# Performance work log

Hardware: AMD Instinct MI355X
Metric: run time of the kernel (lower is better)

The kernel has to match this reference:

```python
import jax, jax.numpy as jnp
import numpy as np

SEQ, D, H, FF = 2048, 1024, 16, 4096
HD = D // H  # head_dim = 64


def setup_inputs() -> dict:
    key = jax.random.key(0)
    ks = jax.random.split(key, 13)
    s = lambda k, shape, fan_in: jax.random.normal(k, shape, jnp.float32) / np.sqrt(fan_in)
    return {
        "x":  jax.random.normal(ks[0], (SEQ, D), jnp.float32),
        # per-head Q/K/V linears, batched over the head axis: [H, D, HD]
        "Wq": s(ks[1], (H, D, HD), D), "bq": jnp.zeros((H, HD), jnp.float32),
        "Wk": s(ks[2], (H, D, HD), D), "bk": jnp.zeros((H, HD), jnp.float32),
        "Wv": s(ks[3], (H, D, HD), D), "bv": jnp.zeros((H, HD), jnp.float32),
        "Wp": s(ks[4], (D, D), D),     "bp": jnp.zeros((D,), jnp.float32),
        "W1": s(ks[5], (D, FF), D),    "b1": jnp.zeros((FF,), jnp.float32),
        "W2": s(ks[6], (FF, D), FF),   "b2": jnp.zeros((D,), jnp.float32),
    }


def reference(x, Wq, bq, Wk, bk, Wv, bv, Wp, bp, W1, b1, W2, b2):
    # Batched per-head projections: [H, S, HD]
    Qx = jnp.einsum("sd,hde->hse", x, Wq) + bq[:, None, :]
    Kx = jnp.einsum("sd,hde->hse", x, Wk) + bk[:, None, :]
    Vx = jnp.einsum("sd,hde->hse", x, Wv) + bv[:, None, :]
    # scores[h,s,t] = Qx[h,s]. Kx[h,t] / sqrt(HD); softmax over t (last dim)
    scores = jnp.einsum("hse,hte->hst", Qx, Kx) / jnp.sqrt(jnp.float32(HD))
    attn = jax.nn.softmax(scores, axis=-1)
    # Faithful to source: head[t,e] = sum_s Vx[s,e] * attn[s,t]  (attn^T @ V)
    heads = jnp.einsum("hse,hst->hte", Vx, attn)  # [H, S, HD]
    # concat heads along feature dim (head-major order) -> [S, D]
    concat = jnp.transpose(heads, (1, 0, 2)).reshape(SEQ, H * HD)
    proj = concat @ Wp + bp
    hidden = jax.nn.relu(proj @ W1 + b1)
    out = hidden @ W2 + b2
    return out
```

## Files before the change

### kernel.cpp

```cpp
#include <hip/hip_runtime.h>
#include <math.h>

constexpr int S_  = 2048;
constexpr int D_  = 1024;
constexpr int H_  = 16;
constexpr int HD_ = 64;
constexpr int FF_ = 4096;

typedef short bf16x8 __attribute__((ext_vector_type(8)));
typedef float f32x4  __attribute__((ext_vector_type(4)));

static __device__ __forceinline__ ushort f2bf(float f) {
    unsigned x = __float_as_uint(f);
    unsigned r = (x + 0x7fffu + ((x >> 16) & 1u)) >> 16;
    return (ushort)r;
}
static __device__ __forceinline__ float bf2f(ushort u) {
    return __uint_as_float(((unsigned)u) << 16);
}

static __device__ __forceinline__ void gload_lds16(const void* g, void* l) {
    __builtin_amdgcn_global_load_lds(
        (const __attribute__((address_space(1))) unsigned int*)g,
        (__attribute__((address_space(3))) unsigned int*)l, 16, 0, 0);
}

__global__ __launch_bounds__(256) void cast_f32_bf16(
    const float* __restrict__ in, ushort* __restrict__ out, int n)
{
    int i = (blockIdx.x * 256 + threadIdx.x) * 4;
    if (i < n) {
        float4 v = *(const float4*)(in + i);
        ushort4 o;
        o.x = f2bf(v.x); o.y = f2bf(v.y); o.z = f2bf(v.z); o.w = f2bf(v.w);
        *(ushort4*)(out + i) = o;
    }
}

__global__ __launch_bounds__(256) void transpose_cast(
    const float* __restrict__ in, ushort* __restrict__ out,
    int K, int N, long inZ, long outZ)
{
    const float* B = in + (size_t)blockIdx.z * inZ;
    ushort* BT = out + (size_t)blockIdx.z * outZ;
    __shared__ float Ts[32][33];
    const int n0 = blockIdx.x * 32, k0 = blockIdx.y * 32;
    const int r = threadIdx.x >> 3, c4 = (threadIdx.x & 7) * 4;
    float4 v = *(const float4*)(B + (size_t)(k0 + r) * N + n0 + c4);
    Ts[r][c4 + 0] = v.x; Ts[r][c4 + 1] = v.y;
    Ts[r][c4 + 2] = v.z; Ts[r][c4 + 3] = v.w;
    __syncthreads();
    ushort4 o;
    o.x = f2bf(Ts[c4 + 0][r]); o.y = f2bf(Ts[c4 + 1][r]);
    o.z = f2bf(Ts[c4 + 2][r]); o.w = f2bf(Ts[c4 + 3][r]);
    *(ushort4*)(BT + (size_t)(n0 + r) * K + k0 + c4) = o;
}

__global__ __launch_bounds__(256) void bias_cat(
    const float* __restrict__ bq, const float* __restrict__ bk,
    const float* __restrict__ bv, float* __restrict__ out)
{
    int i = blockIdx.x * 256 + threadIdx.x;
    float v = (i < 1024) ? bq[i] : (i < 2048 ? bk[i - 1024] : bv[i - 2048]);
    out[i] = v;
}

template <int BM, int BN, int WR, int WC, int KS, int RELU, int OUT>
__global__ __launch_bounds__(WR * WC * 64) void gemm_mfma(
    const ushort* __restrict__ A, const ushort* __restrict__ BT,
    const float* __restrict__ bias, void* __restrict__ Cv,
    void* __restrict__ Cv2, int M, int N, int K)
{
    constexpr int WAVES = WR * WC;
    constexpr int WTM = BM / WR, WTN = BN / WC;
    constexpr int MT = WTM / 16, NT = WTN / 16;
    constexpr int AI = BM / 16;
    constexpr int TI = (BM + BN) / 16;
    constexpr int PW = TI / WAVES;

    __shared__ ushort As[BM * 32];
    __shared__ ushort Bs[BN * 32];

    const int tid = threadIdx.x;
    const int lane = tid & 63;
    const int wave = tid >> 6;
    const int wr = wave / WC, wc = wave % WC;
    const int row16 = lane & 15, kgrp = lane >> 4;
    const int m0 = blockIdx.y * BM, n0 = blockIdx.x * BN;
    const int kOff = blockIdx.z * (K / KS);

    const int lrow = lane >> 2;
    const int gcol8 = (lane & 3) ^ (lrow & 3);
    const int aslot = kgrp ^ (row16 & 3);

    f32x4 acc[MT][NT];
#pragma unroll
    for (int i = 0; i < MT; ++i)
#pragma unroll
        for (int j = 0; j < NT; ++j) acc[i][j] = (f32x4){0.f, 0.f, 0.f, 0.f};

    for (int k0 = kOff; k0 < kOff + K / KS; k0 += 32) {
        __syncthreads();
#pragma unroll
        for (int i = 0; i < PW; ++i) {
            const int inst = wave * PW + i;
            if (inst < AI) {
                const int row = inst * 16 + lrow;
                gload_lds16(A + (size_t)(m0 + row) * K + k0 + gcol8 * 8,
                            As + row * 32 + (lane & 3) * 8);
            } else {
                const int row = (inst - AI) * 16 + lrow;
                gload_lds16(BT + (size_t)(n0 + row) * K + k0 + gcol8 * 8,
                            Bs + row * 32 + (lane & 3) * 8);
            }
        }
        __syncthreads();

        bf16x8 af[MT], bfr[NT];
#pragma unroll
        for (int mt = 0; mt < MT; ++mt)
            af[mt] = *(const bf16x8*)(As + (wr * WTM + mt * 16 + row16) * 32 + aslot * 8);
#pragma unroll
        for (int nt = 0; nt < NT; ++nt)
            bfr[nt] = *(const bf16x8*)(Bs + (wc * WTN + nt * 16 + row16) * 32 + aslot * 8);
#pragma unroll
        for (int mt = 0; mt < MT; ++mt)
#pragma unroll
            for (int nt = 0; nt < NT; ++nt)
                acc[mt][nt] = __builtin_amdgcn_mfma_f32_16x16x32_bf16(
                    af[mt], bfr[nt], acc[mt][nt], 0, 0, 0);
    }

    if constexpr (OUT == 2) {
        float* Cp = ((blockIdx.z < KS / 2) ? (float*)Cv : (float*)Cv2)
                    + (size_t)(blockIdx.z % (KS / 2)) * M * N;
#pragma unroll
        for (int nt = 0; nt < NT; ++nt) {
            const int n = n0 + wc * WTN + nt * 16 + row16;
#pragma unroll
            for (int mt = 0; mt < MT; ++mt)
#pragma unroll
                for (int r = 0; r < 4; ++r) {
                    const int m = m0 + wr * WTM + mt * 16 + kgrp * 4 + r;
                    Cp[(size_t)m * N + n] = acc[mt][nt][r];
                }
        }
    } else if constexpr (OUT == 3) {
        ushort* QKo = (ushort*)Cv;
        ushort* VTo = (ushort*)Cv2;
        if (n0 < 2048) {
#pragma unroll
            for (int nt = 0; nt < NT; ++nt) {
                const int n = n0 + wc * WTN + nt * 16 + row16;
                const float bb = bias[n];
#pragma unroll
                for (int mt = 0; mt < MT; ++mt)
#pragma unroll
                    for (int r = 0; r < 4; ++r) {
                        const int m = m0 + wr * WTM + mt * 16 + kgrp * 4 + r;
                        QKo[(size_t)m * 2048 + n] = f2bf(acc[mt][nt][r] + bb);
                    }
            }
        } else {
#pragma unroll
            for (int nt = 0; nt < NT; ++nt) {
                const int n = n0 + wc * WTN + nt * 16 + row16;
                const float bb = bias[n];
#pragma unroll
                for (int mt = 0; mt < MT; ++mt) {
                    const int mb = m0 + wr * WTM + mt * 16 + kgrp * 4;
                    ushort4 o;
                    o.x = f2bf(acc[mt][nt][0] + bb);
                    o.y = f2bf(acc[mt][nt][1] + bb);
                    o.z = f2bf(acc[mt][nt][2] + bb);
                    o.w = f2bf(acc[mt][nt][3] + bb);
                    *(ushort4*)(VTo + (size_t)(n - 2048) * 2048 + mb) = o;
                }
            }
        }
    } else {
#pragma unroll
        for (int nt = 0; nt < NT; ++nt) {
            const int n = n0 + wc * WTN + nt * 16 + row16;
            const float bb = bias ? bias[n] : 0.f;
#pragma unroll
            for (int mt = 0; mt < MT; ++mt)
#pragma unroll
                for (int r = 0; r < 4; ++r) {
                    const int m = m0 + wr * WTM + mt * 16 + kgrp * 4 + r;
                    float v = acc[mt][nt][r] + bb;
                    if (RELU) v = fmaxf(v, 0.f);
                    if (OUT == 1)
                        ((ushort*)Cv)[(size_t)m * N + n] = f2bf(v);
                    else
                        ((float*)Cv)[(size_t)m * N + n] = v;
                }
        }
    }
}

__global__ __launch_bounds__(256) void reduce4_bias(
    const float* __restrict__ pA, const float* __restrict__ pB,
    const float* __restrict__ bias, float* __restrict__ out, int MN, int N)
{
    const int i = (blockIdx.x * 256 + threadIdx.x) * 4;
    float4 a = *(const float4*)(pA + i);
    const float4 b = *(const float4*)(pA + (size_t)MN + i);
    const float4 c = *(const float4*)(pB + i);
    const float4 d = *(const float4*)(pB + (size_t)MN + i);
    const float4 e = *(const float4*)(bias + (i & (N - 1)));
    a.x += b.x + c.x + d.x + e.x;
    a.y += b.y + c.y + d.y + e.y;
    a.z += b.z + c.z + d.z + e.z;
    a.w += b.w + c.w + d.w + e.w;
    *(float4*)(out + i) = a;
}

__global__ __launch_bounds__(256) void attn_stats(
    const ushort* __restrict__ QK, float* __restrict__ part)
{
    const int h = blockIdx.y;
    const int s0 = blockIdx.x * 128;
    const int tz = blockIdx.z;
    const int tid = threadIdx.x;
    const int lane = tid & 63;
    const int w = tid >> 6;
    const int row16 = lane & 15;
    const int kgrp = lane >> 4;

    __shared__ ushort Ks[64 * 64];

    bf16x8 qf[2][2];
#pragma unroll
    for (int mt = 0; mt < 2; ++mt) {
        const ushort* qp = QK + (size_t)(s0 + w * 32 + mt * 16 + row16) * 2048 + h * 64;
        qf[mt][0] = *(const bf16x8*)(qp + kgrp * 8);
        qf[mt][1] = *(const bf16x8*)(qp + kgrp * 8 + 32);
    }

    float suml[2][4] = {{0.f}};
    const int r0 = tid >> 3, c0 = tid & 7;
    const int sl = (c0 ^ (r0 & 7)) * 8;

    for (int ti = 0; ti < 8; ++ti) {
        const int t0 = tz * 512 + ti * 64;
        uint4 ka = *(const uint4*)(QK + (size_t)(t0 + r0) * 2048 + 1024 + h * 64 + c0 * 8);
        uint4 kb = *(const uint4*)(QK + (size_t)(t0 + 32 + r0) * 2048 + 1024 + h * 64 + c0 * 8);
        __syncthreads();
        *(uint4*)(Ks + r0 * 64 + sl) = ka;
        *(uint4*)(Ks + (r0 + 32) * 64 + sl) = kb;
        __syncthreads();
#pragma unroll
        for (int nt = 0; nt < 4; ++nt) {
            const int kr = nt * 16 + row16;
            bf16x8 kf0 = *(const bf16x8*)(Ks + kr * 64 + ((kgrp ^ (kr & 7)) * 8));
            bf16x8 kf1 = *(const bf16x8*)(Ks + kr * 64 + (((kgrp + 4) ^ (kr & 7)) * 8));
#pragma unroll
            for (int mt = 0; mt < 2; ++mt) {
                f32x4 sc = (f32x4){0.f, 0.f, 0.f, 0.f};
                sc = __builtin_amdgcn_mfma_f32_16x16x32_bf16(qf[mt][0], kf0, sc, 0, 0, 0);
                sc = __builtin_amdgcn_mfma_f32_16x16x32_bf16(qf[mt][1], kf1, sc, 0, 0, 0);
#pragma unroll
                for (int r = 0; r < 4; ++r)
                    suml[mt][r] += __expf(sc[r] * 0.125f);
            }
        }
    }
#pragma unroll
    for (int mt = 0; mt < 2; ++mt)
#pragma unroll
        for (int r = 0; r < 4; ++r) {
#pragma unroll
            for (int m = 1; m < 16; m <<= 1)
                suml[mt][r] += __shfl_xor(suml[mt][r], m, 64);
        }
    if (row16 == 0) {
#pragma unroll
        for (int mt = 0; mt < 2; ++mt)
#pragma unroll
            for (int r = 0; r < 4; ++r)
                part[((size_t)tz * H_ + h) * S_ + s0 + w * 32 + mt * 16 + kgrp * 4 + r]
                    = suml[mt][r];
    }
}

__global__ __launch_bounds__(256) void make_invL(
    const float* __restrict__ part, float* __restrict__ invL)
{
    const int i = blockIdx.x * 256 + threadIdx.x;
    const int HS = H_ * S_;
    float s = part[i] + part[HS + i] + part[2 * HS + i] + part[3 * HS + i];
    invL[i] = 1.f / s;
}

__global__ __launch_bounds__(256) void vscale(
    ushort* __restrict__ VT, const float* __restrict__ invL)
{
    const int r = blockIdx.x;
    const int c = threadIdx.x * 8;
    const float* il = invL + (r >> 6) * S_ + c;
    union { uint4 u; ushort s[8]; } v;
    v.u = *(const uint4*)(VT + (size_t)r * S_ + c);
    float4 l0 = *(const float4*)(il);
    float4 l1 = *(const float4*)(il + 4);
    v.s[0] = f2bf(bf2f(v.s[0]) * l0.x);
    v.s[1] = f2bf(bf2f(v.s[1]) * l0.y);
    v.s[2] = f2bf(bf2f(v.s[2]) * l0.z);
    v.s[3] = f2bf(bf2f(v.s[3]) * l0.w);
    v.s[4] = f2bf(bf2f(v.s[4]) * l1.x);
    v.s[5] = f2bf(bf2f(v.s[5]) * l1.y);
    v.s[6] = f2bf(bf2f(v.s[6]) * l1.z);
    v.s[7] = f2bf(bf2f(v.s[7]) * l1.w);
    *(uint4*)(VT + (size_t)r * S_ + c) = v.u;
}

__global__ __launch_bounds__(256) void attn_pv(
    const ushort* __restrict__ QK, const ushort* __restrict__ VT,
    ushort* __restrict__ pvp)
{
    const int h = blockIdx.y;
    const int t0 = blockIdx.x * 128;
    const int sbase = blockIdx.z * 512;
    const int tid = threadIdx.x;
    const int lane = tid & 63;
    const int w = tid >> 6;
    const int row16 = lane & 15;
    const int kgrp = lane >> 4;

    __shared__ ushort KP[128 * 64];
    __shared__ ushort Qs[64 * 64];
    __shared__ ushort Vs[64 * 64];

    const int r0 = tid >> 3, c0 = tid & 7;
    const int sl = (c0 ^ (r0 & 7)) * 8;

#pragma unroll
    for (int i = 0; i < 4; ++i) {
        const int r = r0 + i * 32;
        uint4 kv = *(const uint4*)(QK + (size_t)(t0 + r) * 2048 + 1024 + h * 64 + c0 * 8);
        *(uint4*)(KP + r * 64 + sl) = kv;
    }
    __syncthreads();
    bf16x8 kf[8][2];
#pragma unroll
    for (int nt = 0; nt < 8; ++nt) {
        const int r = nt * 16 + row16;
        kf[nt][0] = *(const bf16x8*)(KP + r * 64 + ((kgrp ^ (r & 7)) * 8));
        kf[nt][1] = *(const bf16x8*)(KP + r * 64 + (((kgrp + 4) ^ (r & 7)) * 8));
    }

    f32x4 acc[2][4];
#pragma unroll
    for (int i = 0; i < 2; ++i)
#pragma unroll
        for (int j = 0; j < 4; ++j) acc[i][j] = (f32x4){0.f, 0.f, 0.f, 0.f};

    for (int si = 0; si < 8; ++si) {
        const int s0 = sbase + si * 64;
        uint4 qa = *(const uint4*)(QK + (size_t)(s0 + r0) * 2048 + h * 64 + c0 * 8);
        uint4 qb = *(const uint4*)(QK + (size_t)(s0 + 32 + r0) * 2048 + h * 64 + c0 * 8);
        uint4 va = *(const uint4*)(VT + (size_t)(h * 64 + r0) * 2048 + s0 + c0 * 8);
        uint4 vb = *(const uint4*)(VT + (size_t)(h * 64 + 32 + r0) * 2048 + s0 + c0 * 8);
        __syncthreads();
        *(uint4*)(Qs + r0 * 64 + sl) = qa;
        *(uint4*)(Qs + (r0 + 32) * 64 + sl) = qb;
        *(uint4*)(Vs + r0 * 64 + sl) = va;
        *(uint4*)(Vs + (r0 + 32) * 64 + sl) = vb;
        __syncthreads();

        const int qr = w * 16 + row16;
        bf16x8 qf0 = *(const bf16x8*)(Qs + qr * 64 + ((kgrp ^ (qr & 7)) * 8));
        bf16x8 qf1 = *(const bf16x8*)(Qs + qr * 64 + (((kgrp + 4) ^ (qr & 7)) * 8));
#pragma unroll
        for (int nt = 0; nt < 8; ++nt) {
            f32x4 sc = (f32x4){0.f, 0.f, 0.f, 0.f};
            sc = __builtin_amdgcn_mfma_f32_16x16x32_bf16(qf0, kf[nt][0], sc, 0, 0, 0);
            sc = __builtin_amdgcn_mfma_f32_16x16x32_bf16(qf1, kf[nt][1], sc, 0, 0, 0);
            ushort4 o;
            o.x = f2bf(__expf(sc[0] * 0.125f));
            o.y = f2bf(__expf(sc[1] * 0.125f));
            o.z = f2bf(__expf(sc[2] * 0.125f));
            o.w = f2bf(__expf(sc[3] * 0.125f));
            const int tl = nt * 16 + row16;
            const int chunk = w * 2 + (kgrp >> 1);
            *(ushort4*)(KP + tl * 64 + ((chunk ^ (tl & 7)) * 8) + (kgrp & 1) * 4) = o;
        }
        __syncthreads();

        bf16x8 vf[4][2];
#pragma unroll
        for (int nt = 0; nt < 4; ++nt) {
            const int vr = nt * 16 + row16;
            vf[nt][0] = *(const bf16x8*)(Vs + vr * 64 + ((kgrp ^ (vr & 7)) * 8));
            vf[nt][1] = *(const bf16x8*)(Vs + vr * 64 + (((kgrp + 4) ^ (vr & 7)) * 8));
        }
#pragma unroll
        for (int mt = 0; mt < 2; ++mt) {
            const int pr = w * 32 + mt * 16 + row16;
            bf16x8 pf0 = *(const bf16x8*)(KP + pr * 64 + ((kgrp ^ (pr & 7)) * 8));
            bf16x8 pf1 = *(const bf16x8*)(KP + pr * 64 + (((kgrp + 4) ^ (pr & 7)) * 8));
#pragma unroll
            for (int nt = 0; nt < 4; ++nt) {
                acc[mt][nt] = __builtin_amdgcn_mfma_f32_16x16x32_bf16(pf0, vf[nt][0], acc[mt][nt], 0, 0, 0);
                acc[mt][nt] = __builtin_amdgcn_mfma_f32_16x16x32_bf16(pf1, vf[nt][1], acc[mt][nt], 0, 0, 0);
            }
        }
    }

    ushort* dst = pvp + (size_t)blockIdx.z * S_ * D_;
#pragma unroll
    for (int mt = 0; mt < 2; ++mt)
#pragma unroll
        for (int nt = 0; nt < 4; ++nt)
#pragma unroll
            for (int r = 0; r < 4; ++r) {
                const int t = t0 + w * 32 + mt * 16 + kgrp * 4 + r;
                const int e = nt * 16 + row16;
                dst[(size_t)t * D_ + h * 64 + e] = f2bf(acc[mt][nt][r]);
            }
}

__global__ __launch_bounds__(256) void reduce_cat(
    const ushort* __restrict__ p, ushort* __restrict__ concat)
{
    const size_t SD = (size_t)S_ * D_;
    const size_t i = ((size_t)blockIdx.x * 256 + threadIdx.x) * 8;
    union { uint4 u; ushort s[8]; } a, b, c, d, o;
    a.u = *(const uint4*)(p + i);
    b.u = *(const uint4*)(p + SD + i);
    c.u = *(const uint4*)(p + 2 * SD + i);
    d.u = *(const uint4*)(p + 3 * SD + i);
#pragma unroll
    for (int j = 0; j < 8; ++j)
        o.s[j] = f2bf(bf2f(a.s[j]) + bf2f(b.s[j]) + bf2f(c.s[j]) + bf2f(d.s[j]));
    *(uint4*)(concat + i) = o.u;
}

extern "C" void kernel_launch(void* const* d_in, const int* in_sizes, int n_in,
                              void* d_out, int out_size, void* d_ws,
                              size_t ws_size, hipStream_t stream)
{
    const float* x  = (const float*)d_in[0];
    const float* Wq = (const float*)d_in[1];
    const float* bq = (const float*)d_in[2];
    const float* Wk = (const float*)d_in[3];
    const float* bk = (const float*)d_in[4];
    const float* Wv = (const float*)d_in[5];
    const float* bv = (const float*)d_in[6];
    const float* Wp = (const float*)d_in[7];
    const float* bp = (const float*)d_in[8];
    const float* W1 = (const float*)d_in[9];
    const float* b1 = (const float*)d_in[10];
    const float* W2 = (const float*)d_in[11];
    const float* b2 = (const float*)d_in[12];
    float* out = (float*)d_out;

    constexpr size_t MB = 1u << 20;
    char* base = (char*)d_ws;
    ushort* BT2    = (ushort*)(base +  0 * MB);
    ushort* BT1    = (ushort*)(base +  8 * MB);
    ushort* BTp    = (ushort*)(base + 16 * MB);
    ushort* xb     = (ushort*)(base + 18 * MB);
    ushort* concat = (ushort*)(base + 18 * MB);
    ushort* BTqkv  = (ushort*)(base + 22 * MB);
    ushort* projb  = (ushort*)(base + 22 * MB);
    ushort* QKcat  = (ushort*)(base + 28 * MB);
    ushort* hidden = (ushort*)(base + 28 * MB);
    ushort* VTg    = (ushort*)(base + 36 * MB);
    ushort* pvp    = (ushort*)(base + 40 * MB);
    float*  ff2a   = (float*) (base +  8 * MB);
    float*  ff2b   = (float*) (base + 44 * MB);
    float*  biascat= (float*) (base + 60 * MB);
    float*  invL   = biascat + 3072;
    float*  statsP = invL + H_ * S_;

    cast_f32_bf16<<<dim3(S_ * D_ / 1024), 256, 0, stream>>>(x, xb, S_ * D_);
    transpose_cast<<<dim3(HD_ / 32, D_ / 32, H_), 256, 0, stream>>>(
        Wq, BTqkv,               D_, HD_, (long)D_ * HD_, (long)HD_ * D_);
    transpose_cast<<<dim3(HD_ / 32, D_ / 32, H_), 256, 0, stream>>>(
        Wk, BTqkv + 1024 * 1024, D_, HD_, (long)D_ * HD_, (long)HD_ * D_);
    transpose_cast<<<dim3(HD_ / 32, D_ / 32, H_), 256, 0, stream>>>(
        Wv, BTqkv + 2048 * 1024, D_, HD_, (long)D_ * HD_, (long)HD_ * D_);
    transpose_cast<<<dim3(D_ / 32, D_ / 32, 1), 256, 0, stream>>>(
        Wp, BTp, D_, D_, 0, 0);
    transpose_cast<<<dim3(FF_ / 32, D_ / 32, 1), 256, 0, stream>>>(
        W1, BT1, D_, FF_, 0, 0);
    transpose_cast<<<dim3(D_ / 32, FF_ / 32, 1), 256, 0, stream>>>(
        W2, BT2, FF_, D_, 0, 0);
    bias_cat<<<dim3(12), 256, 0, stream>>>(bq, bk, bv, biascat);

    gemm_mfma<128, 128, 2, 2, 1, 0, 3>
        <<<dim3(3072 / 128, S_ / 128, 1), 256, 0, stream>>>(
            xb, BTqkv, biascat, QKcat, VTg, S_, 3072, D_);

    attn_stats<<<dim3(S_ / 128, H_, 4), 256, 0, stream>>>(QKcat, statsP);
    make_invL<<<dim3(H_ * S_ / 256), 256, 0, stream>>>(statsP, invL);

    vscale<<<dim3(D_), 256, 0, stream>>>(VTg, invL);

    attn_pv<<<dim3(S_ / 128, H_, 4), 256, 0, stream>>>(QKcat, VTg, pvp);

    reduce_cat<<<dim3(S_ * D_ / 2048), 256, 0, stream>>>(pvp, concat);

    gemm_mfma<64, 128, 1, 4, 1, 0, 1>
        <<<dim3(D_ / 128, S_ / 64, 1), 256, 0, stream>>>(
            concat, BTp, bp, projb, nullptr, S_, D_, D_);

    gemm_mfma<128, 128, 2, 2, 1, 1, 1>
        <<<dim3(FF_ / 128, S_ / 128, 1), 256, 0, stream>>>(
            projb, BT1, b1, hidden, nullptr, S_, FF_, D_);

    gemm_mfma<128, 128, 2, 2, 4, 0, 2>
        <<<dim3(D_ / 128, S_ / 128, 4), 256, 0, stream>>>(
            hidden, BT2, nullptr, ff2a, ff2b, S_, D_, FF_);

    reduce4_bias<<<dim3(S_ * D_ / 1024), 256, 0, stream>>>(
        ff2a, ff2b, b2, out, S_ * D_, D_);
}
```

Before: 306.9 us.

## Fuse weight packing, deepen GEMM K-tile to 64, fuse vscale, split-K projection

Merges the cast, six transpose_cast launches and the bias concat into one pack_all kernel to cut launch overhead. The GEMM K step grows from 32 to 64, with a larger LDS tile and an XOR swizzle, so there are half as many barriers per K. make_invL is folded into vscale, and the Wp projection becomes split-K by 2 followed by a bias+bf16 reduce kernel. The trade-offs are more LDS per block, an extra reduce pass with fp32 partial traffic for the projection, and f2bf now using the native __bf16 conversion.

```diff
diff --git a/kernel.cpp b/kernel.cpp
--- a/kernel.cpp
+++ b/kernel.cpp
@@ -11,9 +11,9 @@
 typedef float f32x4  __attribute__((ext_vector_type(4)));
 
 static __device__ __forceinline__ ushort f2bf(float f) {
-    unsigned x = __float_as_uint(f);
-    unsigned r = (x + 0x7fffu + ((x >> 16) & 1u)) >> 16;
-    return (ushort)r;
+    union { __bf16 b; ushort u; } c;
+    c.b = (__bf16)f;
+    return c.u;
 }
 static __device__ __forceinline__ float bf2f(ushort u) {
     return __uint_as_float(((unsigned)u) << 16);
@@ -25,44 +25,64 @@
         (__attribute__((address_space(3))) unsigned int*)l, 16, 0, 0);
 }
 
-__global__ __launch_bounds__(256) void cast_f32_bf16(
-    const float* __restrict__ in, ushort* __restrict__ out, int n)
-{
-    int i = (blockIdx.x * 256 + threadIdx.x) * 4;
-    if (i < n) {
-        float4 v = *(const float4*)(in + i);
-        ushort4 o;
-        o.x = f2bf(v.x); o.y = f2bf(v.y); o.z = f2bf(v.z); o.w = f2bf(v.w);
-        *(ushort4*)(out + i) = o;
-    }
-}
-
-__global__ __launch_bounds__(256) void transpose_cast(
+static __device__ __forceinline__ void tc_tile(
     const float* __restrict__ in, ushort* __restrict__ out,
-    int K, int N, long inZ, long outZ)
-{
-    const float* B = in + (size_t)blockIdx.z * inZ;
-    ushort* BT = out + (size_t)blockIdx.z * outZ;
+    int K, int N, int n0, int k0)
+{
     __shared__ float Ts[32][33];
-    const int n0 = blockIdx.x * 32, k0 = blockIdx.y * 32;
-    const int r = threadIdx.x >> 3, c4 = (threadIdx.x & 7) * 4;
-    float4 v = *(const float4*)(B + (size_t)(k0 + r) * N + n0 + c4);
+    const int tid = threadIdx.x;
+    const int r = tid >> 3, c4 = (tid & 7) * 4;
+    float4 v = *(const float4*)(in + (size_t)(k0 + r) * N + n0 + c4);
     Ts[r][c4 + 0] = v.x; Ts[r][c4 + 1] = v.y;
     Ts[r][c4 + 2] = v.z; Ts[r][c4 + 3] = v.w;
     __syncthreads();
     ushort4 o;
     o.x = f2bf(Ts[c4 + 0][r]); o.y = f2bf(Ts[c4 + 1][r]);
     o.z = f2bf(Ts[c4 + 2][r]); o.w = f2bf(Ts[c4 + 3][r]);
-    *(ushort4*)(BT + (size_t)(n0 + r) * K + k0 + c4) = o;
-}
-
-__global__ __launch_bounds__(256) void bias_cat(
+    *(ushort4*)(out + (size_t)(n0 + r) * K + k0 + c4) = o;
+}
+
+__global__ __launch_bounds__(256) void pack_all(
+    const float* __restrict__ x,
+    const float* __restrict__ Wq, const float* __restrict__ Wk,
+    const float* __restrict__ Wv, const float* __restrict__ Wp,
+    const float* __restrict__ W1, const float* __restrict__ W2,
     const float* __restrict__ bq, const float* __restrict__ bk,
-    const float* __restrict__ bv, float* __restrict__ out)
-{
-    int i = blockIdx.x * 256 + threadIdx.x;
-    float v = (i < 1024) ? bq[i] : (i < 2048 ? bk[i - 1024] : bv[i - 2048]);
-    out[i] = v;
+    const float* __restrict__ bv,
+    ushort* __restrict__ xb, ushort* __restrict__ BTqkv,
+    ushort* __restrict__ BTp, ushort* __restrict__ BT1,
+    ushort* __restrict__ BT2, float* __restrict__ biascat)
+{
+    const int b = blockIdx.x;
+    const int tid = threadIdx.x;
+    if (b < 2048) {
+        const int i = b * 1024 + tid * 4;
+        float4 v = *(const float4*)(x + i);
+        ushort4 o;
+        o.x = f2bf(v.x); o.y = f2bf(v.y); o.z = f2bf(v.z); o.w = f2bf(v.w);
+        *(ushort4*)(xb + i) = o;
+    } else if (b < 5120) {
+        int j = b - 2048;
+        const int which = j >> 10;
+        j &= 1023;
+        const int hh = j >> 6, t = j & 63;
+        const float* W = (which == 0) ? Wq : (which == 1) ? Wk : Wv;
+        tc_tile(W + hh * 65536, BTqkv + which * 1024 * 1024 + hh * 65536,
+                1024, 64, (t & 1) * 32, (t >> 1) * 32);
+    } else if (b < 6144) {
+        const int j = b - 5120;
+        tc_tile(Wp, BTp, 1024, 1024, (j & 31) * 32, (j >> 5) * 32);
+    } else if (b < 10240) {
+        const int j = b - 6144;
+        tc_tile(W1, BT1, 1024, 4096, (j & 127) * 32, (j >> 7) * 32);
+    } else if (b < 14336) {
+        const int j = b - 10240;
+        tc_tile(W2, BT2, 4096, 1024, (j & 31) * 32, (j >> 5) * 32);
+    } else {
+        const int i = (b - 14336) * 256 + tid;
+        float v = (i < 1024) ? bq[i] : (i < 2048 ? bk[i - 1024] : bv[i - 2048]);
+        biascat[i] = v;
+    }
 }
 
 template <int BM, int BN, int WR, int WC, int KS, int RELU, int OUT>
@@ -74,12 +94,12 @@
     constexpr int WAVES = WR * WC;
     constexpr int WTM = BM / WR, WTN = BN / WC;
     constexpr int MT = WTM / 16, NT = WTN / 16;
-    constexpr int AI = BM / 16;
-    constexpr int TI = (BM + BN) / 16;
+    constexpr int AI = BM / 8;
+    constexpr int TI = (BM + BN) / 8;
     constexpr int PW = TI / WAVES;
 
-    __shared__ ushort As[BM * 32];
-    __shared__ ushort Bs[BN * 32];
+    __shared__ ushort As[BM * 64];
+    __shared__ ushort Bs[BN * 64];
 
     const int tid = threadIdx.x;
     const int lane = tid & 63;
@@ -87,11 +107,10 @@
     const int wr = wave / WC, wc = wave % WC;
     const int row16 = lane & 15, kgrp = lane >> 4;
     const int m0 = blockIdx.y * BM, n0 = blockIdx.x * BN;
-    const int kOff = blockIdx.z * (K / KS);
-
-    const int lrow = lane >> 2;
-    const int gcol8 = (lane & 3) ^ (lrow & 3);
-    const int aslot = kgrp ^ (row16 & 3);
+    const int kOff = (KS > 1) ? blockIdx.z * (K / KS) : 0;
+
+    const int lrow = lane >> 3;
+    const int sc8 = (lane & 7) ^ lrow;
 
     f32x4 acc[MT][NT];
 #pragma unroll
@@ -99,36 +118,42 @@
 #pragma unroll
         for (int j = 0; j < NT; ++j) acc[i][j] = (f32x4){0.f, 0.f, 0.f, 0.f};
 
-    for (int k0 = kOff; k0 < kOff + K / KS; k0 += 32) {
+    for (int k0 = kOff; k0 < kOff + K / KS; k0 += 64) {
         __syncthreads();
 #pragma unroll
         for (int i = 0; i < PW; ++i) {
             const int inst = wave * PW + i;
             if (inst < AI) {
-                const int row = inst * 16 + lrow;
-                gload_lds16(A + (size_t)(m0 + row) * K + k0 + gcol8 * 8,
-                            As + row * 32 + (lane & 3) * 8);
+                const int row = inst * 8;
+                gload_lds16(A + (size_t)(m0 + row + lrow) * K + k0 + sc8 * 8,
+                            As + row * 64);
             } else {
-                const int row = (inst - AI) * 16 + lrow;
-                gload_lds16(BT + (size_t)(n0 + row) * K + k0 + gcol8 * 8,
-                            Bs + row * 32 + (lane & 3) * 8);
-            }
-        }
-        __syncthreads();
-
-        bf16x8 af[MT], bfr[NT];
-#pragma unroll
-        for (int mt = 0; mt < MT; ++mt)
-            af[mt] = *(const bf16x8*)(As + (wr * WTM + mt * 16 + row16) * 32 + aslot * 8);
-#pragma unroll
-        for (int nt = 0; nt < NT; ++nt)
-            bfr[nt] = *(const bf16x8*)(Bs + (wc * WTN + nt * 16 + row16) * 32 + aslot * 8);
-#pragma unroll
-        for (int mt = 0; mt < MT; ++mt)
-#pragma unroll
-            for (int nt = 0; nt < NT; ++nt)
-                acc[mt][nt] = __builtin_amdgcn_mfma_f32_16x16x32_bf16(
-                    af[mt], bfr[nt], acc[mt][nt], 0, 0, 0);
+                const int row = (inst - AI) * 8;
+                gload_lds16(BT + (size_t)(n0 + row + lrow) * K + k0 + sc8 * 8,
+                            Bs + row * 64);
+            }
+        }
+        __syncthreads();
+#pragma unroll
+        for (int ks = 0; ks < 2; ++ks) {
+            bf16x8 af[MT], bfr[NT];
+#pragma unroll
+            for (int mt = 0; mt < MT; ++mt) {
+                const int r = wr * WTM + mt * 16 + row16;
+                af[mt] = *(const bf16x8*)(As + r * 64 + (((ks * 4 + kgrp) ^ (r & 7)) * 8));
+            }
+#pragma unroll
+            for (int nt = 0; nt < NT; ++nt) {
+                const int r = wc * WTN + nt * 16 + row16;
+                bfr[nt] = *(const bf16x8*)(Bs + r * 64 + (((ks * 4 + kgrp) ^ (r & 7)) * 8));
+            }
+#pragma unroll
+            for (int mt = 0; mt < MT; ++mt)
+#pragma unroll
+                for (int nt = 0; nt < NT; ++nt)
+                    acc[mt][nt] = __builtin_amdgcn_mfma_f32_16x16x32_bf16(
+                        af[mt], bfr[nt], acc[mt][nt], 0, 0, 0);
+        }
     }
 
     if constexpr (OUT == 2) {
@@ -216,6 +241,22 @@
     *(float4*)(out + i) = a;
 }
 
+__global__ __launch_bounds__(256) void reduce2_bias_bf16(
+    const float* __restrict__ pA, const float* __restrict__ pB,
+    const float* __restrict__ bias, ushort* __restrict__ out, int N)
+{
+    const int i = (blockIdx.x * 256 + threadIdx.x) * 4;
+    const float4 a = *(const float4*)(pA + i);
+    const float4 b = *(const float4*)(pB + i);
+    const float4 e = *(const float4*)(bias + (i & (N - 1)));
+    ushort4 o;
+    o.x = f2bf(a.x + b.x + e.x);
+    o.y = f2bf(a.y + b.y + e.y);
+    o.z = f2bf(a.z + b.z + e.z);
+    o.w = f2bf(a.w + b.w + e.w);
+    *(ushort4*)(out + i) = o;
+}
+
 __global__ __launch_bounds__(256) void attn_stats(
     const ushort* __restrict__ QK, float* __restrict__ part)
 {
@@ -284,34 +325,32 @@
     }
 }
 
-__global__ __launch_bounds__(256) void make_invL(
-    const float* __restrict__ part, float* __restrict__ invL)
-{
-    const int i = blockIdx.x * 256 + threadIdx.x;
-    const int HS = H_ * S_;
-    float s = part[i] + part[HS + i] + part[2 * HS + i] + part[3 * HS + i];
-    invL[i] = 1.f / s;
-}
-
-__global__ __launch_bounds__(256) void vscale(
-    ushort* __restrict__ VT, const float* __restrict__ invL)
-{
-    const int r = blockIdx.x;
-    const int c = threadIdx.x * 8;
-    const float* il = invL + (r >> 6) * S_ + c;
-    union { uint4 u; ushort s[8]; } v;
-    v.u = *(const uint4*)(VT + (size_t)r * S_ + c);
-    float4 l0 = *(const float4*)(il);
-    float4 l1 = *(const float4*)(il + 4);
-    v.s[0] = f2bf(bf2f(v.s[0]) * l0.x);
-    v.s[1] = f2bf(bf2f(v.s[1]) * l0.y);
-    v.s[2] = f2bf(bf2f(v.s[2]) * l0.z);
-    v.s[3] = f2bf(bf2f(v.s[3]) * l0.w);
-    v.s[4] = f2bf(bf2f(v.s[4]) * l1.x);
-    v.s[5] = f2bf(bf2f(v.s[5]) * l1.y);
-    v.s[6] = f2bf(bf2f(v.s[6]) * l1.z);
-    v.s[7] = f2bf(bf2f(v.s[7]) * l1.w);
-    *(uint4*)(VT + (size_t)r * S_ + c) = v.u;
+__global__ __launch_bounds__(256) void vscale_fused(
+    ushort* __restrict__ VT, const float* __restrict__ statsP)
+{
+    const int s0 = blockIdx.x * 128;
+    const int h = blockIdx.y;
+    const int tid = threadIdx.x;
+    __shared__ float il[128];
+    if (tid < 128) {
+        const int HS = H_ * S_;
+        const int idx = h * S_ + s0 + tid;
+        float s = statsP[idx] + statsP[HS + idx] +
+                  statsP[2 * HS + idx] + statsP[3 * HS + idx];
+        il[tid] = 1.f / s;
+    }
+    __syncthreads();
+#pragma unroll
+    for (int c = tid; c < 1024; c += 256) {
+        const int row = c >> 4, cc = (c & 15) * 8;
+        const size_t off = (size_t)(h * 64 + row) * 2048 + s0 + cc;
+        union { uint4 u; ushort s[8]; } v;
+        v.u = *(const uint4*)(VT + off);
+#pragma unroll
+        for (int j = 0; j < 8; ++j)
+            v.s[j] = f2bf(bf2f(v.s[j]) * il[cc + j]);
+        *(uint4*)(VT + off) = v.u;
+    }
 }
 
 __global__ __launch_bounds__(256) void attn_pv(
@@ -465,46 +504,37 @@
     ushort* BTqkv  = (ushort*)(base + 22 * MB);
     ushort* projb  = (ushort*)(base + 22 * MB);
     ushort* QKcat  = (ushort*)(base + 28 * MB);
-    ushort* hidden = (ushort*)(base + 28 * MB);
     ushort* VTg    = (ushort*)(base + 36 * MB);
     ushort* pvp    = (ushort*)(base + 40 * MB);
-    float*  ff2a   = (float*) (base +  8 * MB);
-    float*  ff2b   = (float*) (base + 44 * MB);
+    float*  prjA   = (float*) (base + 28 * MB);
+    float*  prjB   = (float*) (base + 36 * MB);
+    ushort* hidden = (ushort*)(base + 28 * MB);
+    float*  ff2a   = (float*) (base + 44 * MB);
+    float*  ff2b   = (float*) (base +  8 * MB);
     float*  biascat= (float*) (base + 60 * MB);
-    float*  invL   = biascat + 3072;
-    float*  statsP = invL + H_ * S_;
-
-    cast_f32_bf16<<<dim3(S_ * D_ / 1024), 256, 0, stream>>>(x, xb, S_ * D_);
-    transpose_cast<<<dim3(HD_ / 32, D_ / 32, H_), 256, 0, stream>>>(
-        Wq, BTqkv,               D_, HD_, (long)D_ * HD_, (long)HD_ * D_);
-    transpose_cast<<<dim3(HD_ / 32, D_ / 32, H_), 256, 0, stream>>>(
-        Wk, BTqkv + 1024 * 1024, D_, HD_, (long)D_ * HD_, (long)HD_ * D_);
-    transpose_cast<<<dim3(HD_ / 32, D_ / 32, H_), 256, 0, stream>>>(
-        Wv, BTqkv + 2048 * 1024, D_, HD_, (long)D_ * HD_, (long)HD_ * D_);
-    transpose_cast<<<dim3(D_ / 32, D_ / 32, 1), 256, 0, stream>>>(
-        Wp, BTp, D_, D_, 0, 0);
-    transpose_cast<<<dim3(FF_ / 32, D_ / 32, 1), 256, 0, stream>>>(
-        W1, BT1, D_, FF_, 0, 0);
-    transpose_cast<<<dim3(D_ / 32, FF_ / 32, 1), 256, 0, stream>>>(
-        W2, BT2, FF_, D_, 0, 0);
-    bias_cat<<<dim3(12), 256, 0, stream>>>(bq, bk, bv, biascat);
+    float*  statsP = biascat + 4096;
+
+    pack_all<<<dim3(14348), 256, 0, stream>>>(
+        x, Wq, Wk, Wv, Wp, W1, W2, bq, bk, bv,
+        xb, BTqkv, BTp, BT1, BT2, biascat);
 
     gemm_mfma<128, 128, 2, 2, 1, 0, 3>
         <<<dim3(3072 / 128, S_ / 128, 1), 256, 0, stream>>>(
             xb, BTqkv, biascat, QKcat, VTg, S_, 3072, D_);
 
     attn_stats<<<dim3(S_ / 128, H_, 4), 256, 0, stream>>>(QKcat, statsP);
-    make_invL<<<dim3(H_ * S_ / 256), 256, 0, stream>>>(statsP, invL);
-
-    vscale<<<dim3(D_), 256, 0, stream>>>(VTg, invL);
+
+    vscale_fused<<<dim3(S_ / 128, H_), 256, 0, stream>>>(VTg, statsP);
 
     attn_pv<<<dim3(S_ / 128, H_, 4), 256, 0, stream>>>(QKcat, VTg, pvp);
 
     reduce_cat<<<dim3(S_ * D_ / 2048), 256, 0, stream>>>(pvp, concat);
 
-    gemm_mfma<64, 128, 1, 4, 1, 0, 1>
-        <<<dim3(D_ / 128, S_ / 64, 1), 256, 0, stream>>>(
-            concat, BTp, bp, projb, nullptr, S_, D_, D_);
+    gemm_mfma<64, 128, 1, 4, 2, 0, 2>
+        <<<dim3(D_ / 128, S_ / 64, 2), 256, 0, stream>>>(
+            concat, BTp, nullptr, prjA, prjB, S_, D_, D_);
+    reduce2_bias_bf16<<<dim3(S_ * D_ / 1024), 256, 0, stream>>>(
+        prjA, prjB, bp, projb, D_);
 
     gemm_mfma<128, 128, 2, 2, 1, 1, 1>
         <<<dim3(FF_ / 128, S_ / 128, 1), 256, 0, stream>>>(
```

After: 274.9 us. 1.12x faster.
